# Kernel tuning notes

Hardware: AMD Instinct MI355X
Metric: run time of the kernel (lower is better)

## Reference

```python
import jax, jax.numpy as jnp
import numpy as np

# ---- module constants (from init_kwargs) ----
EMBED_DIM = 384
NUM_HYPEREDGES = 128
TOPK = 64
SPATIAL_SHAPE = (16, 32, 32)  # D, H, W -> N = 16384
SPACING = (2.0, 1.0, 1.0)
SPATIAL_WEIGHT = 0.1
B, N, C = 4, 16 * 32 * 32, EMBED_DIM


def _l2norm(x, axis=-1, eps=1e-12):
    n = jnp.linalg.norm(x, axis=axis, keepdims=True)
    return x / jnp.maximum(n, eps)


def _get_3d_coords():
    D, H, W = SPATIAL_SHAPE
    z = jnp.arange(D, dtype=jnp.float32) * SPACING[0]
    y = jnp.arange(H, dtype=jnp.float32) * SPACING[1]
    x = jnp.arange(W, dtype=jnp.float32) * SPACING[2]
    zz, yy, xx = jnp.meshgrid(z, y, x, indexing='ij')
    return jnp.stack([zz, yy, xx], axis=-1).reshape(-1, 3)  # (N, 3)


def setup_inputs() -> dict:
    key = jax.random.key(0)
    k1, k2 = jax.random.split(key)
    node_features = jax.random.normal(k1, (B, N, C), dtype=jnp.float32)
    class_token = jax.random.normal(k2, (1, 1, C), dtype=jnp.float32)
    temperature = jnp.ones((1,), dtype=jnp.float32) * 0.07
    return {"node_features": node_features, "class_token": class_token, "temperature": temperature}


def reference(node_features, class_token, temperature):
    Ne = NUM_HYPEREDGES
    w = SPATIAL_WEIGHT
    temp = temperature[0]

    nodes_n = _l2norm(node_features)                      # (B, N, C)

    # Step 1: center sampling by semantic similarity to class token
    ct_n = _l2norm(jnp.broadcast_to(class_token, (B, 1, C)))
    scores = jnp.einsum('boc,bnc->bn', ct_n, nodes_n) / temp  # (B, N)
    _, center_idx = jax.lax.top_k(scores, Ne)             # (B, Ne)

    # Gather centers and compute cosine sim of every center vs all nodes
    centers = jnp.take_along_axis(node_features, center_idx[:, :, None], axis=1)  # (B, Ne, C)
    centers_n = _l2norm(centers)
    sem_sim = jnp.einsum('bec,bnc->ben', centers_n, nodes_n) / temp  # (B, Ne, N)

    # Spatial bias (normalized distance from each center voxel)
    coords = _get_3d_coords()                             # (N, 3)
    center_coords = coords[center_idx]                    # (B, Ne, 3)
    diff = coords[None, None, :, :] - center_coords[:, :, None, :]  # (B, Ne, N, 3)
    dist = jnp.linalg.norm(diff, axis=-1)                 # (B, Ne, N)
    dist = dist / (jnp.max(dist, axis=-1, keepdims=True) + 1e-8)
    combined = (1.0 - w) * sem_sim + w * (1.0 - dist)     # (B, Ne, N)

    # Per-hyperedge top-K neighbors -> incidence matrix H (B, N, Ne)
    _, nbr_idx = jax.lax.top_k(combined, TOPK)            # (B, Ne, K)
    b_ix = jnp.arange(B)[:, None, None]
    e_ix = jnp.arange(Ne)[None, :, None]
    Hmat = jnp.zeros((B, N, Ne), dtype=node_features.dtype)
    Hmat = Hmat.at[b_ix, nbr_idx, e_ix].set(1.0)
    return Hmat
```

## Files before the change

kernel.cpp:

```cpp
#include <hip/hip_runtime.h>
#include <math.h>

#define BB 4
#define NN 16384
#define CC 384
#define NE 128
#define KK 64
#define CAP 1024

typedef unsigned short ushort_t;
typedef __attribute__((ext_vector_type(8))) short bf16x8;
typedef __attribute__((ext_vector_type(4))) float f32x4;
#define MFMA(a, b, c) __builtin_amdgcn_mfma_f32_16x16x32_bf16(a, b, c, 0, 0, 0)

__device__ inline unsigned fkey(float f) {
    unsigned b = __float_as_uint(f);
    return (b & 0x80000000u) ? ~b : (b | 0x80000000u);
}
__device__ inline ushort_t bf16rne(float f) {
    unsigned u = __float_as_uint(f);
    unsigned r = u + 0x7FFFu + ((u >> 16) & 1u);
    return (ushort_t)(r >> 16);
}
__device__ inline float bf16tof(ushort_t h) {
    return __uint_as_float(((unsigned)h) << 16);
}
__device__ inline void cvt2(float fa, float fb, unsigned& hp, unsigned& lp) {
    unsigned ua = __float_as_uint(fa), ub = __float_as_uint(fb);
    unsigned ra = ua + 0x8000u, rb = ub + 0x8000u;
    hp = (ra >> 16) | (rb & 0xFFFF0000u);
    float ha = __uint_as_float(ra & 0xFFFF0000u);
    float hb = __uint_as_float(rb & 0xFFFF0000u);
    float la = fa - ha, lb = fb - hb;
    unsigned lra = __float_as_uint(la) + 0x8000u;
    unsigned lrb = __float_as_uint(lb) + 0x8000u;
    lp = (lra >> 16) | (lrb & 0xFFFF0000u);
}

__device__ inline void load_lds16(const ushort_t* g, ushort_t* l) {
    __builtin_amdgcn_global_load_lds(
        (const __attribute__((address_space(1))) unsigned int*)(const void*)g,
        (__attribute__((address_space(3))) unsigned int*)(void*)l, 16, 0, 0);
}

__device__ inline void bin_select4k(const unsigned* hist, int t, int* wsum,
                                    int* sh_bin, int* sh_r, int r) {
    int base = t * 4;
    int c0 = hist[base], c1 = hist[base + 1], c2 = hist[base + 2], c3 = hist[base + 3];
    int csum = c0 + c1 + c2 + c3;
    int lane = t & 63, wid = t >> 6;
    int x = csum;
#pragma unroll
    for (int off = 1; off < 64; off <<= 1) {
        int v = __shfl_down(x, off, 64);
        if (lane + off < 64) x += v;
    }
    if (lane == 0) wsum[wid] = x;
    __syncthreads();
    int after = 0;
    for (int w2 = wid + 1; w2 < 16; ++w2) after += wsum[w2];
    int S = x - csum + after;
    if (S < r && S + c3 >= r) { *sh_bin = base + 3; *sh_r = r - S; }
    S += c3;
    if (S < r && S + c2 >= r) { *sh_bin = base + 2; *sh_r = r - S; }
    S += c2;
    if (S < r && S + c1 >= r) { *sh_bin = base + 1; *sh_r = r - S; }
    S += c1;
    if (S < r && S + c0 >= r) { *sh_bin = base + 0; *sh_r = r - S; }
    __syncthreads();
}

__global__ __launch_bounds__(256) void k_scores(const float* __restrict__ nf,
                                                const float* __restrict__ ct,
                                                unsigned* __restrict__ keys,
                                                float* __restrict__ invn) {
    int wave = threadIdx.x >> 6;
    int lane = threadIdx.x & 63;
    int row  = blockIdx.x * 4 + wave;
    const float* x = nf + (size_t)row * CC;
    float4 a  = ((const float4*)x)[lane];
    float2 c2 = ((const float2*)(x + 256))[lane];
    float4 ta = ((const float4*)ct)[lane];
    float2 tc = ((const float2*)(ct + 256))[lane];
    float ss = a.x*a.x + a.y*a.y + a.z*a.z + a.w*a.w + c2.x*c2.x + c2.y*c2.y;
    float dt = ta.x*a.x + ta.y*a.y + ta.z*a.z + ta.w*a.w + tc.x*c2.x + tc.y*c2.y;
#pragma unroll
    for (int off = 32; off; off >>= 1) {
        ss += __shfl_xor(ss, off, 64);
        dt += __shfl_xor(dt, off, 64);
    }
    if (lane == 0) {
        float inv = 1.0f / fmaxf(sqrtf(ss), 1e-12f);
        invn[row] = inv;
        keys[row] = fkey(dt * inv);
    }
}

__global__ __launch_bounds__(1024) void k_top128(const unsigned* __restrict__ keys,
                                                 const float* __restrict__ nf,
                                                 const float* __restrict__ invn,
                                                 float* __restrict__ meta,
                                                 ushort_t* __restrict__ Ahi,
                                                 ushort_t* __restrict__ Alo) {
    __shared__ unsigned hist[4096];
    __shared__ int wsum[16];
    __shared__ int sh_bin, sh_r;
    __shared__ unsigned cu[NE];
    __shared__ int cil[NE];
    __shared__ unsigned eqk[CAP];
    __shared__ int eqi[CAP];
    __shared__ int cnt_gt, cnt_eq;
    __shared__ int ocid[NE];
    int b = blockIdx.x;
    int t = threadIdx.x;
    const uint4* rowv = (const uint4*)(keys + b * NN);
    if (t == 0) { cnt_gt = 0; cnt_eq = 0; }
    ((uint4*)hist)[t] = make_uint4(0, 0, 0, 0);
    __syncthreads();
    uint4 u0 = rowv[t], u1 = rowv[t + 1024], u2 = rowv[t + 2048], u3 = rowv[t + 3072];
    atomicAdd(&hist[u0.x >> 20], 1u); atomicAdd(&hist[u0.y >> 20], 1u);
    atomicAdd(&hist[u0.z >> 20], 1u); atomicAdd(&hist[u0.w >> 20], 1u);
    atomicAdd(&hist[u1.x >> 20], 1u); atomicAdd(&hist[u1.y >> 20], 1u);
    atomicAdd(&hist[u1.z >> 20], 1u); atomicAdd(&hist[u1.w >> 20], 1u);
    atomicAdd(&hist[u2.x >> 20], 1u); atomicAdd(&hist[u2.y >> 20], 1u);
    atomicAdd(&hist[u2.z >> 20], 1u); atomicAdd(&hist[u2.w >> 20], 1u);
    atomicAdd(&hist[u3.x >> 20], 1u); atomicAdd(&hist[u3.y >> 20], 1u);
    atomicAdd(&hist[u3.w >> 20], 1u); atomicAdd(&hist[u3.z >> 20], 1u);
    __syncthreads();
    bin_select4k(hist, t, wsum, &sh_bin, &sh_r, NE);
    unsigned bin = (unsigned)sh_bin;
    int r = sh_r;
#define EMIT128(uu, nn) { unsigned tb = (uu) >> 20; \
    if (tb > bin) { int p = atomicAdd(&cnt_gt, 1); cu[p] = (uu); cil[p] = (nn); } \
    else if (tb == bin) { int p = atomicAdd(&cnt_eq, 1); if (p < CAP) { eqk[p] = (uu); eqi[p] = (nn); } } }
    EMIT128(u0.x, 4*t+0); EMIT128(u0.y, 4*t+1); EMIT128(u0.z, 4*t+2); EMIT128(u0.w, 4*t+3);
    EMIT128(u1.x, 4096+4*t+0); EMIT128(u1.y, 4096+4*t+1); EMIT128(u1.z, 4096+4*t+2); EMIT128(u1.w, 4096+4*t+3);
    EMIT128(u2.x, 8192+4*t+0); EMIT128(u2.y, 8192+4*t+1); EMIT128(u2.z, 8192+4*t+2); EMIT128(u2.w, 8192+4*t+3);
    EMIT128(u3.x, 12288+4*t+0); EMIT128(u3.y, 12288+4*t+1); EMIT128(u3.z, 12288+4*t+2); EMIT128(u3.w, 12288+4*t+3);
#undef EMIT128
    __syncthreads();
    int ne = cnt_eq < CAP ? cnt_eq : CAP;
    for (int i = t; i < ne; i += 1024) {
        unsigned ki = eqk[i]; int ii = eqi[i], rk = 0;
        for (int j = 0; j < ne; ++j) {
            unsigned kj = eqk[j];
            rk += (kj > ki) || (kj == ki && eqi[j] < ii);
        }
        if (rk < r) { cu[cnt_gt + rk] = ki; cil[cnt_gt + rk] = ii; }
    }
    __syncthreads();
    if (t < NE) {
        unsigned mu = cu[t]; int mi = cil[t], rk = 0;
#pragma unroll 4
        for (int j = 0; j < NE; ++j) {
            unsigned ou = cu[j]; int oi = cil[j];
            rk += (ou > mu) || (ou == mu && oi < mi);
        }
        ocid[rk] = mi;
    }
    __syncthreads();
    if (t < NE) {
        int ci = ocid[t];
        float zc = (float)(ci >> 10) * 2.0f;
        float yc = (float)((ci >> 5) & 31);
        float xc = (float)(ci & 31);
        float mz = fmaxf(zc * zc, (30.f - zc) * (30.f - zc));
        float my = fmaxf(yc * yc, (31.f - yc) * (31.f - yc));
        float mx = fmaxf(xc * xc, (31.f - xc) * (31.f - xc));
        float md = sqrtf(mz + my + mx);
        int be = b * NE + t;
        meta[be * 4 + 0] = zc;
        meta[be * 4 + 1] = yc;
        meta[be * 4 + 2] = xc;
        meta[be * 4 + 3] = 1.0f / (md + 1e-8f);
    }
    {
        int wid2 = t >> 6, lane2 = t & 63;
        for (int e = wid2; e < NE; e += 16) {
            int ci = ocid[e];
            float inv = invn[b * NN + ci];
            const float* src = nf + ((size_t)b * NN + ci) * CC;
            float4 a  = ((const float4*)src)[lane2];
            float2 cv = ((const float2*)(src + 256))[lane2];
            a.x *= inv; a.y *= inv; a.z *= inv; a.w *= inv;
            cv.x *= inv; cv.y *= inv;
            ushort4 h4; ushort2 h2;
            h4.x = bf16rne(a.x); h4.y = bf16rne(a.y); h4.z = bf16rne(a.z); h4.w = bf16rne(a.w);
            h2.x = bf16rne(cv.x); h2.y = bf16rne(cv.y);
            ushort4 l4; ushort2 l2;
            l4.x = bf16rne(a.x - bf16tof(h4.x)); l4.y = bf16rne(a.y - bf16tof(h4.y));
            l4.z = bf16rne(a.z - bf16tof(h4.z)); l4.w = bf16rne(a.w - bf16tof(h4.w));
            l2.x = bf16rne(cv.x - bf16tof(h2.x)); l2.y = bf16rne(cv.y - bf16tof(h2.y));
            ushort_t* dh = Ahi + ((size_t)b * NE + e) * CC;
            ushort_t* dl = Alo + ((size_t)b * NE + e) * CC;
            ((ushort4*)dh)[lane2] = h4;
            ((ushort2*)(dh + 256))[lane2] = h2;
            ((ushort4*)dl)[lane2] = l4;
            ((ushort2*)(dl + 256))[lane2] = l2;
        }
    }
}

__global__ __launch_bounds__(256, 2) void k_gemm(const float* __restrict__ nf,
                                                 const ushort_t* __restrict__ Ahi,
                                                 const ushort_t* __restrict__ Alo,
                                                 const float* __restrict__ invn,
                                                 const float* __restrict__ meta,
                                                 const float* __restrict__ temp,
                                                 unsigned* __restrict__ outk) {
    __shared__ ushort_t Ah[2][4096], Al[2][4096];
    __shared__ ushort_t Bh[2][4096], Bl[2][4096];
    __shared__ float ms[NE * 4];
    __shared__ float invs_s[128];
    int b  = blockIdx.y;
    int n0 = blockIdx.x * 128;
    int t  = threadIdx.x;
    int w = t >> 6, lane = t & 63, quad = lane >> 4, mrow = lane & 15;
    int wr = w >> 1, wc = w & 1;
    for (int i = t; i < NE * 4; i += 256) ms[i] = meta[b * NE * 4 + i];
    if (t < 128) invs_s[t] = invn[b * NN + n0 + t];
    f32x4 acc[4][4];
#pragma unroll
    for (int i = 0; i < 4; ++i)
#pragma unroll
        for (int j = 0; j < 4; ++j) acc[i][j] = (f32x4)0.f;
    const ushort_t* Abh = Ahi + (size_t)b * NE * CC;
    const ushort_t* Abl = Alo + (size_t)b * NE * CC;
    const ushort_t* gh0 = Abh + (size_t)lane * CC + w * 8;
    const ushort_t* gh1 = Abh + (size_t)(64 + lane) * CC + w * 8;
    const ushort_t* gl0 = Abl + (size_t)lane * CC + w * 8;
    const ushort_t* gl1 = Abl + (size_t)(64 + lane) * CC + w * 8;
    int adst0 = 1024 * w, adst1 = 1024 * w + 512;
    int sb0 = (t & 3) * 128 + (t >> 2);
    int sb1 = sb0 + 64;
    const float* bs0 = nf + ((size_t)b * NN + n0 + (t >> 2)) * CC + (t & 3) * 8;
    const float* bs1 = bs0 + (size_t)64 * CC;
    float4 p0a = ((const float4*)bs0)[0], p0b = ((const float4*)bs0)[1];
    float4 p1a = ((const float4*)bs1)[0], p1b = ((const float4*)bs1)[1];
    load_lds16(gh0, &Ah[0][adst0]);
    load_lds16(gh1, &Ah[0][adst1]);
    load_lds16(gl0, &Al[0][adst0]);
    load_lds16(gl1, &Al[0][adst1]);
    __builtin_amdgcn_sched_barrier(0);
    {
        uint4 ph, pl;
        cvt2(p0a.x, p0a.y, ph.x, pl.x); cvt2(p0a.z, p0a.w, ph.y, pl.y);
        cvt2(p0b.x, p0b.y, ph.z, pl.z); cvt2(p0b.z, p0b.w, ph.w, pl.w);
        *(uint4*)&Bh[0][sb0 * 8] = ph; *(uint4*)&Bl[0][sb0 * 8] = pl;
        cvt2(p1a.x, p1a.y, ph.x, pl.x); cvt2(p1a.z, p1a.w, ph.y, pl.y);
        cvt2(p1b.x, p1b.y, ph.z, pl.z); cvt2(p1b.z, p1b.w, ph.w, pl.w);
        *(uint4*)&Bh[0][sb1 * 8] = ph; *(uint4*)&Bl[0][sb1 * 8] = pl;
    }
    p0a = ((const float4*)(bs0 + 32))[0]; p0b = ((const float4*)(bs0 + 32))[1];
    p1a = ((const float4*)(bs1 + 32))[0]; p1b = ((const float4*)(bs1 + 32))[1];
    asm volatile("s_waitcnt vmcnt(4) lgkmcnt(0)" ::: "memory");
    __builtin_amdgcn_s_barrier();
    __builtin_amdgcn_sched_barrier(0);
    int cur = 0;
    for (int ks = 0; ks < 12; ++ks) {
        int nxt = cur ^ 1;
        if (ks < 11) {
            int kt = (ks + 1) * 32;
            load_lds16(gh0 + kt, &Ah[nxt][adst0]);
            load_lds16(gh1 + kt, &Ah[nxt][adst1]);
            load_lds16(gl0 + kt, &Al[nxt][adst0]);
            load_lds16(gl1 + kt, &Al[nxt][adst1]);
            __builtin_amdgcn_sched_barrier(0);
            uint4 ph, pl;
            cvt2(p0a.x, p0a.y, ph.x, pl.x); cvt2(p0a.z, p0a.w, ph.y, pl.y);
            cvt2(p0b.x, p0b.y, ph.z, pl.z); cvt2(p0b.z, p0b.w, ph.w, pl.w);
            *(uint4*)&Bh[nxt][sb0 * 8] = ph; *(uint4*)&Bl[nxt][sb0 * 8] = pl;
            cvt2(p1a.x, p1a.y, ph.x, pl.x); cvt2(p1a.z, p1a.w, ph.y, pl.y);
            cvt2(p1b.x, p1b.y, ph.z, pl.z); cvt2(p1b.z, p1b.w, ph.w, pl.w);
            *(uint4*)&Bh[nxt][sb1 * 8] = ph; *(uint4*)&Bl[nxt][sb1 * 8] = pl;
            int kt2 = (ks + 2 < 12) ? (ks + 2) * 32 : 0;
            p0a = ((const float4*)(bs0 + kt2))[0]; p0b = ((const float4*)(bs0 + kt2))[1];
            p1a = ((const float4*)(bs1 + kt2))[0]; p1b = ((const float4*)(bs1 + kt2))[1];
        }
        bf16x8 afh[4], afl[4], bfh[4], bfl[4];
#pragma unroll
        for (int i = 0; i < 4; ++i) {
            int m = wr * 64 + i * 16 + mrow;
            afh[i] = *(const bf16x8*)&Ah[cur][(quad * 128 + m) * 8];
            afl[i] = *(const bf16x8*)&Al[cur][(quad * 128 + m) * 8];
        }
#pragma unroll
        for (int j = 0; j < 4; ++j) {
            int n = wc * 64 + j * 16 + mrow;
            bfh[j] = *(const bf16x8*)&Bh[cur][(quad * 128 + n) * 8];
            bfl[j] = *(const bf16x8*)&Bl[cur][(quad * 128 + n) * 8];
        }
#pragma unroll
        for (int i = 0; i < 4; ++i)
#pragma unroll
            for (int j = 0; j < 4; ++j) {
                acc[i][j] = MFMA(afh[i], bfh[j], acc[i][j]);
                acc[i][j] = MFMA(afh[i], bfl[j], acc[i][j]);
                acc[i][j] = MFMA(afl[i], bfh[j], acc[i][j]);
            }
        if (ks < 11) {
            asm volatile("s_waitcnt vmcnt(4) lgkmcnt(0)" ::: "memory");
            __builtin_amdgcn_s_barrier();
            __builtin_amdgcn_sched_barrier(0);
        }
        cur = nxt;
    }
    float scale = 0.9f / temp[0];
#pragma unroll
    for (int j = 0; j < 4; ++j) {
        int nloc = wc * 64 + j * 16 + mrow;
        int n = n0 + nloc;
        float invnn = invs_s[nloc];
        float zf = (float)(n >> 10) * 2.0f;
        float yf = (float)((n >> 5) & 31);
        float xf = (float)(n & 31);
#pragma unroll
        for (int i = 0; i < 4; ++i) {
#pragma unroll
            for (int r = 0; r < 4; ++r) {
                int el = wr * 64 + i * 16 + quad * 4 + r;
                float zc = ms[el * 4 + 0], yc = ms[el * 4 + 1], xc = ms[el * 4 + 2], ivd = ms[el * 4 + 3];
                float dz = zf - zc, dy = yf - yc, dx = xf - xc;
                float dist = sqrtf(dz * dz + dy * dy + dx * dx);
                float v = scale * invnn * acc[i][j][r] + 0.1f * (1.0f - dist * ivd);
                outk[((size_t)(b * NE + el)) * NN + n] = fkey(v);
            }
        }
    }
}

__global__ __launch_bounds__(512) void k_top64(const unsigned* __restrict__ comb,
                                               unsigned* __restrict__ bmg) {
    __shared__ unsigned hist[4096];
    __shared__ unsigned bm[512];
    __shared__ int wsum[8];
    __shared__ int sh_bin, sh_r;
    __shared__ unsigned eqk[CAP];
    __shared__ int eqi[CAP];
    __shared__ int cnt_eq;
    int be = blockIdx.x;
    int t  = threadIdx.x;
    const uint4* rowv = (const uint4*)(comb + (size_t)be * NN);
    if (t == 0) cnt_eq = 0;
    ((uint4*)hist)[t] = make_uint4(0, 0, 0, 0);
    ((uint4*)hist)[t + 512] = make_uint4(0, 0, 0, 0);
    if (t < 128) ((uint4*)bm)[t] = make_uint4(0, 0, 0, 0);
    __syncthreads();
    uint4 u[8];
#pragma unroll
    for (int i = 0; i < 8; ++i) u[i] = rowv[t + 512 * i];
#pragma unroll
    for (int i = 0; i < 8; ++i) {
        atomicAdd(&hist[u[i].x >> 20], 1u); atomicAdd(&hist[u[i].y >> 20], 1u);
        atomicAdd(&hist[u[i].z >> 20], 1u); atomicAdd(&hist[u[i].w >> 20], 1u);
    }
    __syncthreads();
    {
        int base = t * 8;
        int c[8]; int csum = 0;
#pragma unroll
        for (int i = 0; i < 8; ++i) { c[i] = hist[base + i]; csum += c[i]; }
        int lane = t & 63, wid = t >> 6;
        int x = csum;
#pragma unroll
        for (int off = 1; off < 64; off <<= 1) {
            int v = __shfl_down(x, off, 64);
            if (lane + off < 64) x += v;
        }
        if (lane == 0) wsum[wid] = x;
        __syncthreads();
        int after = 0;
        for (int w2 = wid + 1; w2 < 8; ++w2) after += wsum[w2];
        int S = x - csum + after;
#pragma unroll
        for (int i = 7; i >= 0; --i) {
            if (S < KK && S + c[i] >= KK) { sh_bin = base + i; sh_r = KK - S; }
            S += c[i];
        }
        __syncthreads();
    }
    unsigned bin = (unsigned)sh_bin;
    int r = sh_r;
#define EMIT64(uu, nn) { unsigned tb = (uu) >> 20; \
    if (tb > bin) { atomicOr(&bm[(nn) >> 5], 1u << ((nn) & 31)); } \
    else if (tb == bin) { int p = atomicAdd(&cnt_eq, 1); if (p < CAP) { eqk[p] = (uu); eqi[p] = (nn); } } }
#pragma unroll
    for (int i = 0; i < 8; ++i) {
        int nb = 4 * (t + 512 * i);
        EMIT64(u[i].x, nb + 0); EMIT64(u[i].y, nb + 1);
        EMIT64(u[i].z, nb + 2); EMIT64(u[i].w, nb + 3);
    }
#undef EMIT64
    __syncthreads();
    int ne = cnt_eq < CAP ? cnt_eq : CAP;
    for (int i = t; i < ne; i += 512) {
        unsigned ki = eqk[i]; int ii = eqi[i], rk = 0;
        for (int j = 0; j < ne; ++j) {
            unsigned kj = eqk[j];
            rk += (kj > ki) || (kj == ki && eqi[j] < ii);
        }
        if (rk < r) atomicOr(&bm[ii >> 5], 1u << (ii & 31));
    }
    __syncthreads();
    if (t < 128) ((uint4*)(bmg + (size_t)be * 512))[t] = ((uint4*)bm)[t];
}

__global__ __launch_bounds__(256) void k_expand(const unsigned* __restrict__ bmg,
                                                float* __restrict__ H) {
    __shared__ unsigned wl[256];
    int b  = blockIdx.y;
    int n0 = blockIdx.x * 64;
    int t  = threadIdx.x;
    int w0 = n0 >> 5;
    wl[t] = bmg[((size_t)b * NE + (t >> 1)) * 512 + w0 + (t & 1)];
    __syncthreads();
    float4* dst = (float4*)(H + ((size_t)b * NN + n0) * NE);
#pragma unroll
    for (int i = 0; i < 8; ++i) {
        int flat = t + 256 * i;
        int nl = flat >> 5, f4 = flat & 31;
        int wsel = nl >> 5, bit = nl & 31;
        int e = f4 * 4;
        float4 v;
        v.x = (float)((wl[(e + 0) * 2 + wsel] >> bit) & 1u);
        v.y = (float)((wl[(e + 1) * 2 + wsel] >> bit) & 1u);
        v.z = (float)((wl[(e + 2) * 2 + wsel] >> bit) & 1u);
        v.w = (float)((wl[(e + 3) * 2 + wsel] >> bit) & 1u);
        dst[flat] = v;
    }
}

extern "C" void kernel_launch(void* const* d_in, const int* in_sizes, int n_in,
                              void* d_out, int out_size, void* d_ws, size_t ws_size,
                              hipStream_t stream) {
    const float* nf   = (const float*)d_in[0];
    const float* ct   = (const float*)d_in[1];
    const float* temp = (const float*)d_in[2];
    float* out = (float*)d_out;

    unsigned* keys = (unsigned*)d_ws;
    float* invn    = (float*)(keys + BB * NN);
    float* meta    = invn + BB * NN;
    ushort_t* Ahi  = (ushort_t*)(meta + BB * NE * 4);
    ushort_t* Alo  = Ahi + (size_t)BB * NE * CC;
    unsigned* bmg  = (unsigned*)(Alo + (size_t)BB * NE * CC);

    k_scores <<<BB * NN / 4, 256, 0, stream>>>(nf, ct, keys, invn);
    k_top128 <<<BB, 1024, 0, stream>>>(keys, nf, invn, meta, Ahi, Alo);
    k_gemm   <<<dim3(NN / 128, BB), 256, 0, stream>>>(nf, Ahi, Alo, invn, meta, temp, (unsigned*)out);
    k_top64  <<<BB * NE, 512, 0, stream>>>((const unsigned*)out, bmg);
    k_expand <<<dim3(NN / 64, BB), 256, 0, stream>>>(bmg, out);
}
```

Measured before the change: 234.4 us.

## Pre-tile center matrix layout, pad B LDS, deepen prefetch and unroll GEMM loop

The centers kernel now writes the hi/lo bf16 center matrices in a k-chunk-major tiled layout, so each GEMM wave's A-tile load is one contiguous 16-byte-per-lane read instead of a row-strided one. The B tiles in LDS are padded (stride 130 instead of 128) to reduce bank conflicts on the fragment reads. The node-feature register prefetch is deepened to two k-steps ahead, and the k loop is fully unrolled with s_setprio raised around the MFMA block. The cost is more registers held for prefetch and larger code, which may pressure occupancy under the launch bounds of 2 blocks per CU.

```diff
diff --git a/kernel.cpp b/kernel.cpp
--- a/kernel.cpp
+++ b/kernel.cpp
@@ -125,7 +125,7 @@
     atomicAdd(&hist[u2.x >> 20], 1u); atomicAdd(&hist[u2.y >> 20], 1u);
     atomicAdd(&hist[u2.z >> 20], 1u); atomicAdd(&hist[u2.w >> 20], 1u);
     atomicAdd(&hist[u3.x >> 20], 1u); atomicAdd(&hist[u3.y >> 20], 1u);
-    atomicAdd(&hist[u3.w >> 20], 1u); atomicAdd(&hist[u3.z >> 20], 1u);
+    atomicAdd(&hist[u3.z >> 20], 1u); atomicAdd(&hist[u3.w >> 20], 1u);
     __syncthreads();
     bin_select4k(hist, t, wsum, &sh_bin, &sh_r, NE);
     unsigned bin = (unsigned)sh_bin;
@@ -176,6 +176,8 @@
     }
     {
         int wid2 = t >> 6, lane2 = t & 63;
+        ushort_t* dh = Ahi + (size_t)b * NE * CC;
+        ushort_t* dl = Alo + (size_t)b * NE * CC;
         for (int e = wid2; e < NE; e += 16) {
             int ci = ocid[e];
             float inv = invn[b * NN + ci];
@@ -191,12 +193,12 @@
             l4.x = bf16rne(a.x - bf16tof(h4.x)); l4.y = bf16rne(a.y - bf16tof(h4.y));
             l4.z = bf16rne(a.z - bf16tof(h4.z)); l4.w = bf16rne(a.w - bf16tof(h4.w));
             l2.x = bf16rne(cv.x - bf16tof(h2.x)); l2.y = bf16rne(cv.y - bf16tof(h2.y));
-            ushort_t* dh = Ahi + ((size_t)b * NE + e) * CC;
-            ushort_t* dl = Alo + ((size_t)b * NE + e) * CC;
-            ((ushort4*)dh)[lane2] = h4;
-            ((ushort2*)(dh + 256))[lane2] = h2;
-            ((ushort4*)dl)[lane2] = l4;
-            ((ushort2*)(dl + 256))[lane2] = l2;
+            int off4 = ((lane2 >> 1) * NE + e) * 8 + 4 * (lane2 & 1);
+            int off2 = ((32 + (lane2 >> 2)) * NE + e) * 8 + 2 * (lane2 & 3);
+            *(ushort4*)(dh + off4) = h4;
+            *(ushort2*)(dh + off2) = h2;
+            *(ushort4*)(dl + off4) = l4;
+            *(ushort2*)(dl + off2) = l2;
         }
     }
 }
@@ -209,7 +211,7 @@
                                                  const float* __restrict__ temp,
                                                  unsigned* __restrict__ outk) {
     __shared__ ushort_t Ah[2][4096], Al[2][4096];
-    __shared__ ushort_t Bh[2][4096], Bl[2][4096];
+    __shared__ ushort_t Bh[2][4160], Bl[2][4160];
     __shared__ float ms[NE * 4];
     __shared__ float invs_s[128];
     int b  = blockIdx.y;
@@ -226,85 +228,102 @@
         for (int j = 0; j < 4; ++j) acc[i][j] = (f32x4)0.f;
     const ushort_t* Abh = Ahi + (size_t)b * NE * CC;
     const ushort_t* Abl = Alo + (size_t)b * NE * CC;
-    const ushort_t* gh0 = Abh + (size_t)lane * CC + w * 8;
-    const ushort_t* gh1 = Abh + (size_t)(64 + lane) * CC + w * 8;
-    const ushort_t* gl0 = Abl + (size_t)lane * CC + w * 8;
-    const ushort_t* gl1 = Abl + (size_t)(64 + lane) * CC + w * 8;
-    int adst0 = 1024 * w, adst1 = 1024 * w + 512;
-    int sb0 = (t & 3) * 128 + (t >> 2);
-    int sb1 = sb0 + 64;
-    const float* bs0 = nf + ((size_t)b * NN + n0 + (t >> 2)) * CC + (t & 3) * 8;
+    const ushort_t* ah0 = Abh + w * 1024 + lane * 8;
+    const ushort_t* ah1 = ah0 + 512;
+    const ushort_t* al0 = Abl + w * 1024 + lane * 8;
+    const ushort_t* al1 = al0 + 512;
+    int bn = t >> 2, bk8 = t & 3;
+    int sb0 = bk8 * 130 + bn, sb1 = sb0 + 64;
+    const float* bs0 = nf + ((size_t)b * NN + n0 + bn) * CC + bk8 * 8;
     const float* bs1 = bs0 + (size_t)64 * CC;
-    float4 p0a = ((const float4*)bs0)[0], p0b = ((const float4*)bs0)[1];
-    float4 p1a = ((const float4*)bs1)[0], p1b = ((const float4*)bs1)[1];
-    load_lds16(gh0, &Ah[0][adst0]);
-    load_lds16(gh1, &Ah[0][adst1]);
-    load_lds16(gl0, &Al[0][adst0]);
-    load_lds16(gl1, &Al[0][adst1]);
+    float4 s0a, s0b, s0c, s0d;
+    float4 s1a, s1b, s1c, s1d;
+    load_lds16(ah0, &Ah[0][w * 1024]);
+    load_lds16(ah1, &Ah[0][w * 1024 + 512]);
+    load_lds16(al0, &Al[0][w * 1024]);
+    load_lds16(al1, &Al[0][w * 1024 + 512]);
     __builtin_amdgcn_sched_barrier(0);
+    s0a = ((const float4*)bs0)[0]; s0b = ((const float4*)bs0)[1];
+    s0c = ((const float4*)bs1)[0]; s0d = ((const float4*)bs1)[1];
+    s1a = ((const float4*)(bs0 + 32))[0]; s1b = ((const float4*)(bs0 + 32))[1];
+    s1c = ((const float4*)(bs1 + 32))[0]; s1d = ((const float4*)(bs1 + 32))[1];
     {
         uint4 ph, pl;
-        cvt2(p0a.x, p0a.y, ph.x, pl.x); cvt2(p0a.z, p0a.w, ph.y, pl.y);
-        cvt2(p0b.x, p0b.y, ph.z, pl.z); cvt2(p0b.z, p0b.w, ph.w, pl.w);
+        cvt2(s0a.x, s0a.y, ph.x, pl.x); cvt2(s0a.z, s0a.w, ph.y, pl.y);
+        cvt2(s0b.x, s0b.y, ph.z, pl.z); cvt2(s0b.z, s0b.w, ph.w, pl.w);
         *(uint4*)&Bh[0][sb0 * 8] = ph; *(uint4*)&Bl[0][sb0 * 8] = pl;
-        cvt2(p1a.x, p1a.y, ph.x, pl.x); cvt2(p1a.z, p1a.w, ph.y, pl.y);
-        cvt2(p1b.x, p1b.y, ph.z, pl.z); cvt2(p1b.z, p1b.w, ph.w, pl.w);
+        cvt2(s0c.x, s0c.y, ph.x, pl.x); cvt2(s0c.z, s0c.w, ph.y, pl.y);
+        cvt2(s0d.x, s0d.y, ph.z, pl.z); cvt2(s0d.z, s0d.w, ph.w, pl.w);
         *(uint4*)&Bh[0][sb1 * 8] = ph; *(uint4*)&Bl[0][sb1 * 8] = pl;
     }
-    p0a = ((const float4*)(bs0 + 32))[0]; p0b = ((const float4*)(bs0 + 32))[1];
-    p1a = ((const float4*)(bs1 + 32))[0]; p1b = ((const float4*)(bs1 + 32))[1];
-    asm volatile("s_waitcnt vmcnt(4) lgkmcnt(0)" ::: "memory");
+    s0a = ((const float4*)(bs0 + 64))[0]; s0b = ((const float4*)(bs0 + 64))[1];
+    s0c = ((const float4*)(bs1 + 64))[0]; s0d = ((const float4*)(bs1 + 64))[1];
+    asm volatile("s_waitcnt vmcnt(8) lgkmcnt(0)" ::: "memory");
     __builtin_amdgcn_s_barrier();
     __builtin_amdgcn_sched_barrier(0);
-    int cur = 0;
-    for (int ks = 0; ks < 12; ++ks) {
-        int nxt = cur ^ 1;
-        if (ks < 11) {
-            int kt = (ks + 1) * 32;
-            load_lds16(gh0 + kt, &Ah[nxt][adst0]);
-            load_lds16(gh1 + kt, &Ah[nxt][adst1]);
-            load_lds16(gl0 + kt, &Al[nxt][adst0]);
-            load_lds16(gl1 + kt, &Al[nxt][adst1]);
-            __builtin_amdgcn_sched_barrier(0);
-            uint4 ph, pl;
-            cvt2(p0a.x, p0a.y, ph.x, pl.x); cvt2(p0a.z, p0a.w, ph.y, pl.y);
-            cvt2(p0b.x, p0b.y, ph.z, pl.z); cvt2(p0b.z, p0b.w, ph.w, pl.w);
-            *(uint4*)&Bh[nxt][sb0 * 8] = ph; *(uint4*)&Bl[nxt][sb0 * 8] = pl;
-            cvt2(p1a.x, p1a.y, ph.x, pl.x); cvt2(p1a.z, p1a.w, ph.y, pl.y);
-            cvt2(p1b.x, p1b.y, ph.z, pl.z); cvt2(p1b.z, p1b.w, ph.w, pl.w);
-            *(uint4*)&Bh[nxt][sb1 * 8] = ph; *(uint4*)&Bl[nxt][sb1 * 8] = pl;
-            int kt2 = (ks + 2 < 12) ? (ks + 2) * 32 : 0;
-            p0a = ((const float4*)(bs0 + kt2))[0]; p0b = ((const float4*)(bs0 + kt2))[1];
-            p1a = ((const float4*)(bs1 + kt2))[0]; p1b = ((const float4*)(bs1 + kt2))[1];
-        }
-        bf16x8 afh[4], afl[4], bfh[4], bfl[4];
-#pragma unroll
-        for (int i = 0; i < 4; ++i) {
-            int m = wr * 64 + i * 16 + mrow;
-            afh[i] = *(const bf16x8*)&Ah[cur][(quad * 128 + m) * 8];
-            afl[i] = *(const bf16x8*)&Al[cur][(quad * 128 + m) * 8];
-        }
-#pragma unroll
-        for (int j = 0; j < 4; ++j) {
-            int n = wc * 64 + j * 16 + mrow;
-            bfh[j] = *(const bf16x8*)&Bh[cur][(quad * 128 + n) * 8];
-            bfl[j] = *(const bf16x8*)&Bl[cur][(quad * 128 + n) * 8];
-        }
-#pragma unroll
-        for (int i = 0; i < 4; ++i)
-#pragma unroll
-            for (int j = 0; j < 4; ++j) {
-                acc[i][j] = MFMA(afh[i], bfh[j], acc[i][j]);
-                acc[i][j] = MFMA(afh[i], bfl[j], acc[i][j]);
-                acc[i][j] = MFMA(afl[i], bfh[j], acc[i][j]);
-            }
-        if (ks < 11) {
-            asm volatile("s_waitcnt vmcnt(4) lgkmcnt(0)" ::: "memory");
-            __builtin_amdgcn_s_barrier();
-            __builtin_amdgcn_sched_barrier(0);
-        }
-        cur = nxt;
-    }
+
+#define GSTEP(KS, CUR, NXT, SA, SB, SC, SD)                                     \
+    {                                                                           \
+        if ((KS) < 11) {                                                        \
+            const int kt = ((KS) + 1) * 32;                                     \
+            load_lds16(ah0 + kt * 128, &Ah[NXT][w * 1024]);                     \
+            load_lds16(ah1 + kt * 128, &Ah[NXT][w * 1024 + 512]);               \
+            load_lds16(al0 + kt * 128, &Al[NXT][w * 1024]);                     \
+            load_lds16(al1 + kt * 128, &Al[NXT][w * 1024 + 512]);               \
+            __builtin_amdgcn_sched_barrier(0);                                  \
+            uint4 ph, pl;                                                       \
+            cvt2(SA.x, SA.y, ph.x, pl.x); cvt2(SA.z, SA.w, ph.y, pl.y);         \
+            cvt2(SB.x, SB.y, ph.z, pl.z); cvt2(SB.z, SB.w, ph.w, pl.w);         \
+            *(uint4*)&Bh[NXT][sb0 * 8] = ph; *(uint4*)&Bl[NXT][sb0 * 8] = pl;   \
+            cvt2(SC.x, SC.y, ph.x, pl.x); cvt2(SC.z, SC.w, ph.y, pl.y);         \
+            cvt2(SD.x, SD.y, ph.z, pl.z); cvt2(SD.z, SD.w, ph.w, pl.w);         \
+            *(uint4*)&Bh[NXT][sb1 * 8] = ph; *(uint4*)&Bl[NXT][sb1 * 8] = pl;   \
+            const int kt3 = ((KS) + 3 <= 11 ? (KS) + 3 : 11) * 32;              \
+            SA = ((const float4*)(bs0 + kt3))[0];                               \
+            SB = ((const float4*)(bs0 + kt3))[1];                               \
+            SC = ((const float4*)(bs1 + kt3))[0];                               \
+            SD = ((const float4*)(bs1 + kt3))[1];                               \
+        }                                                                       \
+        bf16x8 afh[4], afl[4], bfh[4], bfl[4];                                  \
+        _Pragma("unroll") for (int i = 0; i < 4; ++i) {                         \
+            int m = wr * 64 + i * 16 + mrow;                                    \
+            afh[i] = *(const bf16x8*)&Ah[CUR][(quad * 128 + m) * 8];            \
+            afl[i] = *(const bf16x8*)&Al[CUR][(quad * 128 + m) * 8];            \
+        }                                                                       \
+        _Pragma("unroll") for (int j = 0; j < 4; ++j) {                         \
+            int n = wc * 64 + j * 16 + mrow;                                    \
+            bfh[j] = *(const bf16x8*)&Bh[CUR][(quad * 130 + n) * 8];            \
+            bfl[j] = *(const bf16x8*)&Bl[CUR][(quad * 130 + n) * 8];            \
+        }                                                                       \
+        __builtin_amdgcn_s_setprio(1);                                          \
+        _Pragma("unroll") for (int i = 0; i < 4; ++i)                           \
+        _Pragma("unroll") for (int j = 0; j < 4; ++j) {                         \
+            acc[i][j] = MFMA(afh[i], bfh[j], acc[i][j]);                        \
+            acc[i][j] = MFMA(afh[i], bfl[j], acc[i][j]);                        \
+            acc[i][j] = MFMA(afl[i], bfh[j], acc[i][j]);                        \
+        }                                                                       \
+        __builtin_amdgcn_s_setprio(0);                                          \
+        if ((KS) < 11) {                                                        \
+            asm volatile("s_waitcnt vmcnt(4) lgkmcnt(0)" ::: "memory");         \
+            __builtin_amdgcn_s_barrier();                                       \
+            __builtin_amdgcn_sched_barrier(0);                                  \
+        }                                                                       \
+    }
+
+    GSTEP(0, 0, 1, s1a, s1b, s1c, s1d)
+    GSTEP(1, 1, 0, s0a, s0b, s0c, s0d)
+    GSTEP(2, 0, 1, s1a, s1b, s1c, s1d)
+    GSTEP(3, 1, 0, s0a, s0b, s0c, s0d)
+    GSTEP(4, 0, 1, s1a, s1b, s1c, s1d)
+    GSTEP(5, 1, 0, s0a, s0b, s0c, s0d)
+    GSTEP(6, 0, 1, s1a, s1b, s1c, s1d)
+    GSTEP(7, 1, 0, s0a, s0b, s0c, s0d)
+    GSTEP(8, 0, 1, s1a, s1b, s1c, s1d)
+    GSTEP(9, 1, 0, s0a, s0b, s0c, s0d)
+    GSTEP(10, 0, 1, s1a, s1b, s1c, s1d)
+    GSTEP(11, 1, 0, s0a, s0b, s0c, s0d)
+#undef GSTEP
+
     float scale = 0.9f / temp[0];
 #pragma unroll
     for (int j = 0; j < 4; ++j) {
```

Result: slower. 242.6 us (+3.5%).
